# Optimization experiments

Hardware: AMD Instinct MI355X
Metric: run time of the kernel (lower is better)

Reference implementation:

```python
import jax, jax.numpy as jnp
import numpy as np
from jax import lax

DN2 = ('NCHW', 'OIHW', 'NCHW')
DN3 = ('NCDHW', 'OIDHW', 'NCDHW')


def _convlstm_step(h, c, x, W, b):
    # x: [B, Cin, H, W], h/c: [B, nf, H, W], W: [4*nf, Cin+nf, 3, 3]
    comb = jnp.concatenate([x, h], axis=1)
    cc = lax.conv_general_dilated(comb, W, (1, 1), 'SAME', dimension_numbers=DN2)
    cc = cc + b[None, :, None, None]
    ci, cf, co, cg = jnp.split(cc, 4, axis=1)
    i = jax.nn.sigmoid(ci)
    f = jax.nn.sigmoid(cf)
    o = jax.nn.sigmoid(co)
    g = jnp.tanh(cg)
    c_next = f * c + i * g
    h_next = o * jnp.tanh(c_next)
    return h_next, c_next


def setup_inputs() -> dict:
    key = jax.random.key(0)
    ks = jax.random.split(key, 4)
    B, T, Cin, H, W = 32, 12, 1, 64, 64
    nf = 64
    s = 0.05
    return {
        'x': jax.random.normal(ks[0], (B, T, Cin, H, W), jnp.float32),
        'future_step': 12,
        'W_enc': jax.random.normal(ks[1], (4 * nf, Cin + nf, 3, 3), jnp.float32) * s,
        'b_enc': jnp.zeros((4 * nf,), jnp.float32),
        'W_dec': jax.random.normal(ks[2], (4 * nf, nf + nf, 3, 3), jnp.float32) * s,
        'b_dec': jnp.zeros((4 * nf,), jnp.float32),
        'W_cnn': jax.random.normal(ks[3], (1, nf, 1, 3, 3), jnp.float32) * s,
        'b_cnn': jnp.zeros((1,), jnp.float32),
    }


def reference(x, future_step, W_enc, b_enc, W_dec, b_dec, W_cnn, b_cnn):
    B, T, Cin, H, Wd = x.shape
    nf = W_enc.shape[0] // 4
    h0 = jnp.zeros((B, nf, H, Wd), x.dtype)
    c0 = jnp.zeros((B, nf, H, Wd), x.dtype)

    # ---- encoder: scan over time ----
    def enc_step(carry, xt):
        h, c = carry
        h, c = _convlstm_step(h, c, xt, W_enc, b_enc)
        return (h, c), None

    (h_t, _), _ = lax.scan(enc_step, (h0, c0), jnp.moveaxis(x, 1, 0))
    encoder_vector = h_t
    out_encoder_vector = encoder_vector.reshape(B, -1)

    # ---- decoder: feed back h as next input ----
    def dec_step(carry, _):
        ev, h, c = carry
        h, c = _convlstm_step(h, c, ev, W_dec, b_dec)
        return (h, h, c), h

    _, outs = lax.scan(dec_step, (encoder_vector, h0, c0), None, length=future_step)
    # outs: [Tf, B, nf, H, W] -> [B, nf, Tf, H, W]
    outs = jnp.transpose(outs, (1, 2, 0, 3, 4))

    # ---- 3D CNN head: kernel (1,3,3), padding (0,1,1) ----
    y = lax.conv_general_dilated(outs, W_cnn, (1, 1, 1),
                                 [(0, 0), (1, 1), (1, 1)],
                                 dimension_numbers=DN3)
    y = y + b_cnn[None, :, None, None, None]
    # [B, 1, Tf, H, W] -> [B, Tf, 1, H, W]
    y = jnp.transpose(y, (0, 2, 1, 3, 4))
    return y, out_encoder_vector
```

## Files before the change

kernel.cpp:

```cpp
#include <hip/hip_runtime.h>
#include <hip/hip_bf16.h>


#define HW 4096
#define NF 64

typedef __attribute__((ext_vector_type(8))) short bf16x8;
typedef __attribute__((ext_vector_type(4))) float f32x4;

__device__ __forceinline__ float fsig(float v) {
  return __builtin_amdgcn_rcpf(1.f + __expf(-v));
}
__device__ __forceinline__ float ftanh(float v) {
  float vc = fminf(fmaxf(v, -15.f), 15.f);
  float e = __expf(2.f * vc);
  return (e - 1.f) * __builtin_amdgcn_rcpf(e + 1.f);
}
__device__ __forceinline__ float bf2f(short s) {
  union { unsigned u; float f; } a;
  a.u = ((unsigned)(unsigned short)s) << 16;
  return a.f;
}
__device__ __forceinline__ short f2bf(float f) {
  union { float f; unsigned u; } a;
  a.f = f;
  unsigned r = (a.u + 0x7fff + ((a.u >> 16) & 1)) >> 16;
  return (short)r;
}
__device__ __forceinline__ void dma16(const short* g, short* l) {
  __builtin_amdgcn_global_load_lds(
      (const __attribute__((address_space(1))) char*)g,
      (__attribute__((address_space(3))) char*)l, 16, 0, 0);
}

template <bool HAS_X, bool HAS_H, bool FUSE_HEAD>
__global__ __launch_bounds__(512) void lstm_mfma_k(
    const short* __restrict__ hin,
    const short* __restrict__ W,
    const float* __restrict__ wx,
    const float* __restrict__ xpl,
    const float* __restrict__ bias,
    const float* __restrict__ cin,
    const short* __restrict__ zbuf,
    short* __restrict__ hout,
    float* __restrict__ cout,
    const float* __restrict__ wc2,
    const float* __restrict__ bcnn,
    float* __restrict__ yout,
    int th) {
  if (FUSE_HEAD) {
    if (blockIdx.x >= 32) {
      const int f = ((blockIdx.x - 32) * 64 + blockIdx.y) * 512 + threadIdx.x;
      const int pix = f & 4095;
      const int b = f >> 12;
      const int x0 = pix & 63, y0 = pix >> 6;
      float acc = bcnn[0];
      const short* hb = hin + (size_t)b * (HW * 64);
#pragma unroll
      for (int tap = 0; tap < 9; ++tap) {
        const int yy = y0 + tap / 3 - 1, xx = x0 + (tap % 3) - 1;
        if (yy < 0 || yy > 63 || xx < 0 || xx > 63) continue;
        const short* hp = hb + (yy * 64 + xx) * 64;
        const int sw8 = (xx + 1) & 7;
        const float* wp = wc2 + tap * 64;
#pragma unroll
        for (int f8 = 0; f8 < 8; ++f8) {
          bf16x8 v = *reinterpret_cast<const bf16x8*>(hp + ((f8 ^ sw8) * 8));
#pragma unroll
          for (int j = 0; j < 8; ++j)
            acc = fmaf(wp[f8 * 8 + j], bf2f(v[j]), acc);
        }
      }
      yout[(size_t)(b * 12 + th) * HW + pix] = acc;
      return;
    }
  }
  const int b = blockIdx.x;
  const int y = blockIdx.y;
  const int tid = threadIdx.x;
  const int lane = tid & 63;
  const int wv = tid >> 6;
  const int wnf = wv & 3;
  const int whalf = wv >> 2;
  const int col = lane & 15;
  const int quad = lane >> 4;

  __shared__ short As3[3][8192];
  __shared__ short Bs[3 * 66 * 64];
  __shared__ float xs[3][64];

  if (HAS_H) {
    const short* hb = hin + (size_t)b * (HW * 64);
#pragma unroll
    for (int r = 0; r < 3; ++r) {
      const int py = y - 1 + r;
      const short* src = (py >= 0 && py < 64)
          ? hb + ((py * 64 + 8 * wv + (lane >> 3)) * 64 + (lane & 7) * 8)
          : zbuf + lane * 8;
      dma16(src, &Bs[(r * 66 + 8 * wv + 1) * 64]);
    }
#pragma unroll
    for (int k = 0; k < 2; ++k) {
      const short* src = W + (k >> 1) * 16384 + (k & 1) * 8192;
      dma16(src + (wv * 64 + lane) * 8, &As3[k][wv * 64 * 8]);
      dma16(src + (512 + wv * 64 + lane) * 8, &As3[k][(512 + wv * 64) * 8]);
    }
    if (tid < 48) {
      const int r = tid >> 4;
      const int s = ((tid >> 3) & 1) * 65;
      const int ch0 = (tid & 7) * 8;
      bf16x8 z = {0, 0, 0, 0, 0, 0, 0, 0};
      *reinterpret_cast<bf16x8*>(&Bs[(r * 66 + s) * 64 + ch0]) = z;
    }
  }
  if (HAS_X) {
    if (tid < 192) {
      const float* xb = xpl + (size_t)b * (12 * HW);
      const int r = tid >> 6, cx = tid & 63;
      const int py = y - 1 + r;
      xs[r][cx] = (py >= 0 && py < 64) ? xb[py * 64 + cx] : 0.f;
    }
  }
  if (HAS_H) {
    asm volatile("s_waitcnt vmcnt(2) lgkmcnt(0)" ::: "memory");
    __builtin_amdgcn_s_barrier();
  } else {
    __syncthreads();
  }

  f32x4 acc[4][2];
#pragma unroll
  for (int g = 0; g < 4; ++g) {
    const int oc0 = g * 64 + wnf * 16 + quad * 4;
#pragma unroll
    for (int nt = 0; nt < 2; ++nt)
#pragma unroll
      for (int r = 0; r < 4; ++r) acc[g][nt][r] = bias[oc0 + r];
  }

  if (HAS_X) {
#pragma unroll
    for (int tap = 0; tap < 9; ++tap) {
      float xv[2];
#pragma unroll
      for (int nt = 0; nt < 2; ++nt) {
        const int pxx = whalf * 32 + nt * 16 + col + (tap % 3) - 1;
        xv[nt] = (pxx >= 0 && pxx < 64) ? xs[tap / 3][pxx] : 0.f;
      }
      const float* wt = wx + tap * 256;
#pragma unroll
      for (int g = 0; g < 4; ++g) {
        const int oc0 = g * 64 + wnf * 16 + quad * 4;
        const f32x4 w4 = *reinterpret_cast<const f32x4*>(wt + oc0);
#pragma unroll
        for (int nt = 0; nt < 2; ++nt)
#pragma unroll
          for (int r = 0; r < 4; ++r)
            acc[g][nt][r] = fmaf(xv[nt], w4[r], acc[g][nt][r]);
      }
    }
  }

  if (HAS_H) {
    const int axr = (col & 7) << 3;
    bf16x8 bh00, bh01, bh10, bh11;
#pragma unroll
    for (int k = 0; k < 18; ++k) {
      const int tap = k >> 1, gp = k & 1, p = k % 3;
      if (k > 0) {
        if (k == 17)
          asm volatile("s_waitcnt vmcnt(0)" ::: "memory");
        else
          asm volatile("s_waitcnt vmcnt(2)" ::: "memory");
        __builtin_amdgcn_s_barrier();
      }
      if (k + 2 < 18) {
        const int nk = k + 2;
        const short* src = W + (nk >> 1) * 16384 + (nk & 1) * 8192;
        dma16(src + (wv * 64 + lane) * 8, &As3[nk % 3][wv * 64 * 8]);
        dma16(src + (512 + wv * 64 + lane) * 8,
              &As3[nk % 3][(512 + wv * 64) * 8]);
      }
      if (gp == 0) {
        const int hr = tap / 3;
        const int sb = col + tap % 3;
        const int sx = (sb & 7) << 3;
        const int srow = (hr * 66 + whalf * 32 + sb) * 64;
        const int b0 = (srow + quad * 8) ^ sx;
        const int b1 = (srow + 32 + quad * 8) ^ sx;
        bh00 = *reinterpret_cast<const bf16x8*>(&Bs[b0]);
        bh01 = *reinterpret_cast<const bf16x8*>(&Bs[b0 + 1024]);
        bh10 = *reinterpret_cast<const bf16x8*>(&Bs[b1]);
        bh11 = *reinterpret_cast<const bf16x8*>(&Bs[b1 + 1024]);
      }
#pragma unroll
      for (int kc = 0; kc < 2; ++kc) {
        const int chb = kc * 32 + quad * 8;
        const int abase = ((wnf * 16 + col) * 64 + chb) ^ axr;
        bf16x8 a0 = *reinterpret_cast<const bf16x8*>(&As3[p][abase]);
        bf16x8 a1 = *reinterpret_cast<const bf16x8*>(&As3[p][abase + 4096]);
        const bf16x8 bb0 = kc ? bh10 : bh00;
        const bf16x8 bb1 = kc ? bh11 : bh01;
        __builtin_amdgcn_s_setprio(1);
        acc[gp * 2][0] = __builtin_amdgcn_mfma_f32_16x16x32_bf16(a0, bb0, acc[gp * 2][0], 0, 0, 0);
        acc[gp * 2][1] = __builtin_amdgcn_mfma_f32_16x16x32_bf16(a0, bb1, acc[gp * 2][1], 0, 0, 0);
        acc[gp * 2 + 1][0] = __builtin_amdgcn_mfma_f32_16x16x32_bf16(a1, bb0, acc[gp * 2 + 1][0], 0, 0, 0);
        acc[gp * 2 + 1][1] = __builtin_amdgcn_mfma_f32_16x16x32_bf16(a1, bb1, acc[gp * 2 + 1][1], 0, 0, 0);
        __builtin_amdgcn_s_setprio(0);
      }
    }
  }

  const int nf0 = wnf * 16 + quad * 4;
#pragma unroll
  for (int nt = 0; nt < 2; ++nt) {
    const int px = whalf * 32 + nt * 16 + col;
    const int swz = ((px + 1) & 7) << 3;
    const size_t pix = (size_t)b * HW + y * 64 + px;
    f32x4 cold = {0.f, 0.f, 0.f, 0.f};
    if (cin) cold = *reinterpret_cast<const f32x4*>(cin + pix * 64 + nf0);
    f32x4 cnew;
    short hnew[4];
#pragma unroll
    for (int r = 0; r < 4; ++r) {
      float i_ = fsig(acc[0][nt][r]);
      float f_ = fsig(acc[1][nt][r]);
      float o_ = fsig(acc[2][nt][r]);
      float g_ = ftanh(acc[3][nt][r]);
      float cn = fmaf(f_, cold[r], i_ * g_);
      cnew[r] = cn;
      hnew[r] = f2bf(o_ * ftanh(cn));
    }
    *reinterpret_cast<f32x4*>(cout + pix * 64 + nf0) = cnew;
    short4 hv = make_short4(hnew[0], hnew[1], hnew[2], hnew[3]);
    *reinterpret_cast<short4*>(hout + pix * 64 + (nf0 ^ swz)) = hv;
  }
}

__global__ __launch_bounds__(256) void head_k(const short* __restrict__ h,
                                              const float* __restrict__ wc2,
                                              const float* __restrict__ bc,
                                              float* __restrict__ yout, int t) {
  const int tid = blockIdx.x * 256 + threadIdx.x;
  const int pix = tid & 4095;
  const int b = tid >> 12;
  const int x0 = pix & 63, y0 = pix >> 6;
  float acc = bc[0];
  const short* hb = h + (size_t)b * (HW * 64);
#pragma unroll
  for (int tap = 0; tap < 9; ++tap) {
    const int yy = y0 + tap / 3 - 1, xx = x0 + (tap % 3) - 1;
    if (yy < 0 || yy > 63 || xx < 0 || xx > 63) continue;
    const short* hp = hb + (yy * 64 + xx) * 64;
    const int sw8 = (xx + 1) & 7;
    const float* wp = wc2 + tap * 64;
#pragma unroll
    for (int f8 = 0; f8 < 8; ++f8) {
      bf16x8 v = *reinterpret_cast<const bf16x8*>(hp + ((f8 ^ sw8) * 8));
#pragma unroll
      for (int j = 0; j < 8; ++j) acc = fmaf(wp[f8 * 8 + j], bf2f(v[j]), acc);
    }
  }
  yout[(size_t)(b * 12 + t) * HW + pix] = acc;
}

__global__ __launch_bounds__(256) void ev_out_k(const short* __restrict__ h,
                                                float* __restrict__ out) {
  __shared__ float tl[64][65];
  const int b = blockIdx.y, pg = blockIdx.x;
  const int p0 = pg * 64;
  {
    const int pixl = threadIdx.x >> 2, c0 = (threadIdx.x & 3) * 16;
    const int sw8 = (pixl + 1) & 7;
    const short* hp = h + ((size_t)b * HW + p0 + pixl) * 64;
#pragma unroll
    for (int gi = 0; gi < 2; ++gi) {
      const int grp = (c0 >> 3) + gi;
      bf16x8 v = *reinterpret_cast<const bf16x8*>(hp + ((grp ^ sw8) * 8));
#pragma unroll
      for (int j = 0; j < 8; ++j) tl[pixl][grp * 8 + j] = bf2f(v[j]);
    }
  }
  __syncthreads();
  {
    const int ch = threadIdx.x >> 2, q0 = (threadIdx.x & 3) * 16;
    float* op = out + ((size_t)b * 64 + ch) * (size_t)HW + p0 + q0;
#pragma unroll
    for (int i = 0; i < 16; ++i) op[i] = tl[q0 + i][ch];
  }
}

__global__ __launch_bounds__(256) void reo_enc_k(const float* __restrict__ src,
                                                 short* __restrict__ Wh,
                                                 float* __restrict__ wx) {
  const int idx = blockIdx.x * 256 + threadIdx.x;
  if (idx < 9 * 256 * 64) {
    const int tap = idx >> 14, oc = (idx >> 6) & 255, c = idx & 63;
    const int dst = tap * 16384 + (((oc * 64) + c) ^ ((oc & 7) << 3));
    Wh[dst] = f2bf(src[(oc * 65 + (c + 1)) * 9 + tap]);
  }
  if (idx < 256 * 9) {
    const int tap = idx >> 8, oc = idx & 255;
    wx[idx] = src[(oc * 65 + 0) * 9 + tap];
  }
}

__global__ __launch_bounds__(256) void reo_dec_k(const float* __restrict__ src,
                                                 short* __restrict__ Wx,
                                                 short* __restrict__ Ws) {
  const int idx = blockIdx.x * 256 + threadIdx.x;
  if (idx >= 9 * 256 * 64) return;
  const int tap = idx >> 14, oc = (idx >> 6) & 255, c = idx & 63;
  const int dst = tap * 16384 + (((oc * 64) + c) ^ ((oc & 7) << 3));
  const float a = src[(oc * 128 + c) * 9 + tap];
  const float b = src[(oc * 128 + 64 + c) * 9 + tap];
  Wx[dst] = f2bf(a);
  Ws[dst] = f2bf(a + b);
}

__global__ __launch_bounds__(256) void reo_cnn_k(const float* __restrict__ src,
                                                 float* __restrict__ wc2) {
  const int idx = blockIdx.x * 256 + threadIdx.x;
  if (idx >= 576) return;
  wc2[idx] = src[(idx % 64) * 9 + (idx / 64)];
}

extern "C" void kernel_launch(void* const* d_in, const int* in_sizes, int n_in,
                              void* d_out, int out_size, void* d_ws, size_t ws_size,
                              hipStream_t stream) {
  const float* x = (const float*)d_in[0];
  const float* W_enc = (const float*)d_in[2];
  const float* b_enc = (const float*)d_in[3];
  const float* W_dec = (const float*)d_in[4];
  const float* b_dec = (const float*)d_in[5];
  const float* W_cnn = (const float*)d_in[6];
  const float* b_cnn = (const float*)d_in[7];
  float* out = (float*)d_out;
  float* out_y = out;
  float* out_ev = out + 1572864;

  float* ws = (float*)d_ws;
  float* cA = ws;
  float* cB = cA + 8388608;
  short* hA = (short*)(cB + 8388608);
  short* hB = hA + 8388608;
  short* WEh = hB + 8388608;
  short* WDx = WEh + 147456;
  short* WDs = WDx + 147456;
  float* wx = (float*)(WDs + 147456);
  float* wc2 = wx + 2304;
  short* zb = (short*)(wc2 + 576);

  reo_enc_k<<<(147456 + 255) / 256, 256, 0, stream>>>(W_enc, WEh, wx);
  reo_dec_k<<<(147456 + 255) / 256, 256, 0, stream>>>(W_dec, WDx, WDs);
  reo_cnn_k<<<3, 256, 0, stream>>>(W_cnn, wc2);
  hipMemsetAsync(zb, 0, 512 * sizeof(short), stream);

  dim3 gridL(32, 64), blkL(512);
  dim3 gridF(36, 64);
  dim3 gridE(64, 32), blkE(256);

  lstm_mfma_k<true, false, false><<<gridL, blkL, 0, stream>>>(
      nullptr, WEh, wx, x, b_enc, nullptr, zb, hB, cB,
      nullptr, nullptr, nullptr, 0);
  short *ha = hB, *hb = hA;
  float *ca = cB, *cb = cA;

  for (int t = 1; t < 12; ++t) {
    lstm_mfma_k<true, true, false><<<gridL, blkL, 0, stream>>>(
        ha, WEh, wx, x + t * HW, b_enc, ca, zb, hb, cb,
        nullptr, nullptr, nullptr, 0);
    { short* tm = ha; ha = hb; hb = tm; }
    { float* tm = ca; ca = cb; cb = tm; }
  }
  ev_out_k<<<gridE, blkE, 0, stream>>>(ha, out_ev);

  lstm_mfma_k<false, true, false><<<gridL, blkL, 0, stream>>>(
      ha, WDx, nullptr, nullptr, b_dec, nullptr, zb, hb, cb,
      nullptr, nullptr, nullptr, 0);
  { short* tm = ha; ha = hb; hb = tm; }
  { float* tm = ca; ca = cb; cb = tm; }

  for (int t = 1; t < 12; ++t) {
    lstm_mfma_k<false, true, true><<<gridF, blkL, 0, stream>>>(
        ha, WDs, nullptr, nullptr, b_dec, ca, zb, hb, cb,
        wc2, b_cnn, out_y, t - 1);
    { short* tm = ha; ha = hb; hb = tm; }
    { float* tm = ca; ca = cb; cb = tm; }
  }
  head_k<<<512, 256, 0, stream>>>(ha, wc2, b_cnn, out_y, 11);
}
```

Before: 1.815 ms.

## Process eight output rows per block with a rolling h-row ring buffer

Each recurrent LSTM block now computes 8 consecutive image rows instead of 1. It keeps a 4-slot ring buffer of h rows (and x rows) in shared memory, so each input row is loaded once and reused across three output rows rather than reloaded three times. Weight tiles keep streaming through the triple buffer across rows. The grid shrinks from 2048 to 256 blocks, plus 256 head blocks in the fused variant, which cuts redundant halo loads and launch overhead but may leave CUs underused on a 256-CU device. The weights are re-streamed for every row, and the first timestep is split into its own path.

Result: slower. 2.939 ms (+62.0%).

```diff
diff --git a/kernel.cpp b/kernel.cpp
--- a/kernel.cpp
+++ b/kernel.cpp
@@ -48,9 +48,10 @@
     const float* __restrict__ bcnn,
     float* __restrict__ yout,
     int th) {
+  const int tid = threadIdx.x;
   if (FUSE_HEAD) {
-    if (blockIdx.x >= 32) {
-      const int f = ((blockIdx.x - 32) * 64 + blockIdx.y) * 512 + threadIdx.x;
+    if (blockIdx.y >= 8) {
+      const int f = (blockIdx.x + (blockIdx.y - 8) * 32) * 512 + tid;
       const int pix = f & 4095;
       const int b = f >> 12;
       const int x0 = pix & 63, y0 = pix >> 6;
@@ -76,8 +77,6 @@
     }
   }
   const int b = blockIdx.x;
-  const int y = blockIdx.y;
-  const int tid = threadIdx.x;
   const int lane = tid & 63;
   const int wv = tid >> 6;
   const int wnf = wv & 3;
@@ -86,59 +85,27 @@
   const int quad = lane >> 4;
 
   __shared__ short As3[3][8192];
-  __shared__ short Bs[3 * 66 * 64];
-  __shared__ float xs[3][64];
-
-  if (HAS_H) {
-    const short* hb = hin + (size_t)b * (HW * 64);
-#pragma unroll
-    for (int r = 0; r < 3; ++r) {
-      const int py = y - 1 + r;
-      const short* src = (py >= 0 && py < 64)
-          ? hb + ((py * 64 + 8 * wv + (lane >> 3)) * 64 + (lane & 7) * 8)
-          : zbuf + lane * 8;
-      dma16(src, &Bs[(r * 66 + 8 * wv + 1) * 64]);
-    }
-#pragma unroll
-    for (int k = 0; k < 2; ++k) {
-      const short* src = W + (k >> 1) * 16384 + (k & 1) * 8192;
-      dma16(src + (wv * 64 + lane) * 8, &As3[k][wv * 64 * 8]);
-      dma16(src + (512 + wv * 64 + lane) * 8, &As3[k][(512 + wv * 64) * 8]);
-    }
-    if (tid < 48) {
-      const int r = tid >> 4;
-      const int s = ((tid >> 3) & 1) * 65;
-      const int ch0 = (tid & 7) * 8;
-      bf16x8 z = {0, 0, 0, 0, 0, 0, 0, 0};
-      *reinterpret_cast<bf16x8*>(&Bs[(r * 66 + s) * 64 + ch0]) = z;
-    }
-  }
-  if (HAS_X) {
+  __shared__ short Bs[4][4224];
+  __shared__ float xs[4][64];
+
+  if (!HAS_H) {
+    const int y = blockIdx.y;
     if (tid < 192) {
       const float* xb = xpl + (size_t)b * (12 * HW);
       const int r = tid >> 6, cx = tid & 63;
       const int py = y - 1 + r;
       xs[r][cx] = (py >= 0 && py < 64) ? xb[py * 64 + cx] : 0.f;
     }
-  }
-  if (HAS_H) {
-    asm volatile("s_waitcnt vmcnt(2) lgkmcnt(0)" ::: "memory");
-    __builtin_amdgcn_s_barrier();
-  } else {
     __syncthreads();
-  }
-
-  f32x4 acc[4][2];
-#pragma unroll
-  for (int g = 0; g < 4; ++g) {
-    const int oc0 = g * 64 + wnf * 16 + quad * 4;
-#pragma unroll
-    for (int nt = 0; nt < 2; ++nt)
-#pragma unroll
-      for (int r = 0; r < 4; ++r) acc[g][nt][r] = bias[oc0 + r];
-  }
-
-  if (HAS_X) {
+    f32x4 acc[4][2];
+#pragma unroll
+    for (int g = 0; g < 4; ++g) {
+      const int oc0 = g * 64 + wnf * 16 + quad * 4;
+#pragma unroll
+      for (int nt = 0; nt < 2; ++nt)
+#pragma unroll
+        for (int r = 0; r < 4; ++r) acc[g][nt][r] = bias[oc0 + r];
+    }
 #pragma unroll
     for (int tap = 0; tap < 9; ++tap) {
       float xv[2];
@@ -159,46 +126,156 @@
             acc[g][nt][r] = fmaf(xv[nt], w4[r], acc[g][nt][r]);
       }
     }
-  }
-
-  if (HAS_H) {
-    const int axr = (col & 7) << 3;
+    const int nf0 = wnf * 16 + quad * 4;
+#pragma unroll
+    for (int nt = 0; nt < 2; ++nt) {
+      const int px = whalf * 32 + nt * 16 + col;
+      const int swz = ((px + 1) & 7) << 3;
+      const size_t pix = (size_t)b * HW + y * 64 + px;
+      f32x4 cnew;
+      short hnew[4];
+#pragma unroll
+      for (int r = 0; r < 4; ++r) {
+        float i_ = fsig(acc[0][nt][r]);
+        float o_ = fsig(acc[2][nt][r]);
+        float g_ = ftanh(acc[3][nt][r]);
+        float cn = i_ * g_;
+        cnew[r] = cn;
+        hnew[r] = f2bf(o_ * ftanh(cn));
+      }
+      *reinterpret_cast<f32x4*>(cout + pix * 64 + nf0) = cnew;
+      short4 hv = make_short4(hnew[0], hnew[1], hnew[2], hnew[3]);
+      *reinterpret_cast<short4*>(hout + pix * 64 + (nf0 ^ swz)) = hv;
+    }
+    return;
+  }
+
+  const int y0 = blockIdx.y * 8;
+  const short* hb = hin + (size_t)b * (HW * 64);
+  const float* xb = HAS_X ? (xpl + (size_t)b * (12 * HW)) : nullptr;
+
+#pragma unroll
+  for (int r = 0; r < 3; ++r) {
+    const int py = y0 - 1 + r;
+    const short* src = (py >= 0)
+        ? hb + ((py * 64 + 8 * wv + (lane >> 3)) * 64 + (lane & 7) * 8)
+        : zbuf + lane * 8;
+    dma16(src, &Bs[(py + 1) & 3][64 + wv * 512]);
+  }
+#pragma unroll
+  for (int k = 0; k < 2; ++k) {
+    const short* src = W + k * 8192;
+    dma16(src + (wv * 64 + lane) * 8, &As3[k][wv * 64 * 8]);
+    dma16(src + (512 + wv * 64 + lane) * 8, &As3[k][(512 + wv * 64) * 8]);
+  }
+  if (tid < 64) {
+    const int rs = tid >> 4, s = ((tid >> 3) & 1) * 65, ch0 = (tid & 7) * 8;
+    bf16x8 z = {0, 0, 0, 0, 0, 0, 0, 0};
+    *reinterpret_cast<bf16x8*>(&Bs[rs][s * 64 + ch0]) = z;
+  }
+  if (HAS_X) {
+    if (tid < 192) {
+      const int r = tid >> 6, cx = tid & 63;
+      const int py = y0 - 1 + r;
+      xs[(py + 1) & 3][cx] = (py >= 0) ? xb[py * 64 + cx] : 0.f;
+    }
+  }
+  asm volatile("s_waitcnt vmcnt(0) lgkmcnt(0)" ::: "memory");
+  __builtin_amdgcn_s_barrier();
+
+  const int axr = (col & 7) << 3;
+  const int abase0 = ((wnf * 16 + col) * 64 + quad * 8) ^ axr;
+  const int abase1 = ((wnf * 16 + col) * 64 + 32 + quad * 8) ^ axr;
+  short* BsF = &Bs[0][0];
+
+#pragma unroll 1
+  for (int r = 0; r < 8; ++r) {
+    const int y = y0 + r;
+    f32x4 acc[4][2];
+#pragma unroll
+    for (int g = 0; g < 4; ++g) {
+      const int oc0 = g * 64 + wnf * 16 + quad * 4;
+#pragma unroll
+      for (int nt = 0; nt < 2; ++nt)
+#pragma unroll
+        for (int q = 0; q < 4; ++q) acc[g][nt][q] = bias[oc0 + q];
+    }
+    if (HAS_X) {
+#pragma unroll
+      for (int tap = 0; tap < 9; ++tap) {
+        const float* xrow = xs[(y + tap / 3) & 3];
+        float xv[2];
+#pragma unroll
+        for (int nt = 0; nt < 2; ++nt) {
+          const int pxx = whalf * 32 + nt * 16 + col + (tap % 3) - 1;
+          xv[nt] = (pxx >= 0 && pxx < 64) ? xrow[pxx] : 0.f;
+        }
+        const float* wt = wx + tap * 256;
+#pragma unroll
+        for (int g = 0; g < 4; ++g) {
+          const int oc0 = g * 64 + wnf * 16 + quad * 4;
+          const f32x4 w4 = *reinterpret_cast<const f32x4*>(wt + oc0);
+#pragma unroll
+          for (int nt = 0; nt < 2; ++nt)
+#pragma unroll
+            for (int q = 0; q < 4; ++q)
+              acc[g][nt][q] = fmaf(xv[nt], w4[q], acc[g][nt][q]);
+        }
+      }
+    }
+    const int rb[3] = {((y) & 3) * 4224, ((y + 1) & 3) * 4224,
+                       ((y + 2) & 3) * 4224};
     bf16x8 bh00, bh01, bh10, bh11;
-#pragma unroll
-    for (int k = 0; k < 18; ++k) {
-      const int tap = k >> 1, gp = k & 1, p = k % 3;
-      if (k > 0) {
-        if (k == 17)
-          asm volatile("s_waitcnt vmcnt(0)" ::: "memory");
-        else
-          asm volatile("s_waitcnt vmcnt(2)" ::: "memory");
+
+#pragma unroll
+    for (int j = 0; j < 18; ++j) {
+      const int tap = j >> 1, gp = j & 1;
+      if (j == 0) {
         __builtin_amdgcn_s_barrier();
-      }
-      if (k + 2 < 18) {
-        const int nk = k + 2;
-        const short* src = W + (nk >> 1) * 16384 + (nk & 1) * 8192;
-        dma16(src + (wv * 64 + lane) * 8, &As3[nk % 3][wv * 64 * 8]);
+        {
+          const int py = y + 2;
+          const short* srcB = (py <= 63)
+              ? hb + ((py * 64 + 8 * wv + (lane >> 3)) * 64 + (lane & 7) * 8)
+              : zbuf + lane * 8;
+          dma16(srcB, &Bs[(py + 1) & 3][64 + wv * 512]);
+          if (HAS_X) {
+            const short* srcX = (py <= 63)
+                ? reinterpret_cast<const short*>(xb + py * 64 + wv * 8) +
+                      lane * 8
+                : zbuf + lane * 8;
+            if (lane < 2)
+              dma16(srcX, reinterpret_cast<short*>(&xs[(py + 1) & 3][wv * 8]));
+          }
+        }
+      } else if (j == 1) {
+        __builtin_amdgcn_s_barrier();
+      } else {
+        asm volatile("s_waitcnt vmcnt(2)" ::: "memory");
+        __builtin_amdgcn_s_barrier();
+      }
+      {
+        const int p2 = (j + 2) % 18;
+        const short* src = W + (p2 >> 1) * 16384 + (p2 & 1) * 8192;
+        dma16(src + (wv * 64 + lane) * 8, &As3[(j + 2) % 3][wv * 64 * 8]);
         dma16(src + (512 + wv * 64 + lane) * 8,
-              &As3[nk % 3][(512 + wv * 64) * 8]);
+              &As3[(j + 2) % 3][(512 + wv * 64) * 8]);
       }
       if (gp == 0) {
         const int hr = tap / 3;
         const int sb = col + tap % 3;
         const int sx = (sb & 7) << 3;
-        const int srow = (hr * 66 + whalf * 32 + sb) * 64;
-        const int b0 = (srow + quad * 8) ^ sx;
-        const int b1 = (srow + 32 + quad * 8) ^ sx;
-        bh00 = *reinterpret_cast<const bf16x8*>(&Bs[b0]);
-        bh01 = *reinterpret_cast<const bf16x8*>(&Bs[b0 + 1024]);
-        bh10 = *reinterpret_cast<const bf16x8*>(&Bs[b1]);
-        bh11 = *reinterpret_cast<const bf16x8*>(&Bs[b1 + 1024]);
+        const int o = rb[hr] + (whalf * 32 + sb) * 64;
+        bh00 = *reinterpret_cast<const bf16x8*>(&BsF[(o + quad * 8) ^ sx]);
+        bh01 = *reinterpret_cast<const bf16x8*>(&BsF[(o + 1024 + quad * 8) ^ sx]);
+        bh10 = *reinterpret_cast<const bf16x8*>(&BsF[(o + 32 + quad * 8) ^ sx]);
+        bh11 = *reinterpret_cast<const bf16x8*>(&BsF[(o + 1024 + 32 + quad * 8) ^ sx]);
       }
 #pragma unroll
       for (int kc = 0; kc < 2; ++kc) {
-        const int chb = kc * 32 + quad * 8;
-        const int abase = ((wnf * 16 + col) * 64 + chb) ^ axr;
-        bf16x8 a0 = *reinterpret_cast<const bf16x8*>(&As3[p][abase]);
-        bf16x8 a1 = *reinterpret_cast<const bf16x8*>(&As3[p][abase + 4096]);
+        const bf16x8 a0 = *reinterpret_cast<const bf16x8*>(
+            &As3[j % 3][kc ? abase1 : abase0]);
+        const bf16x8 a1 = *reinterpret_cast<const bf16x8*>(
+            &As3[j % 3][(kc ? abase1 : abase0) + 4096]);
         const bf16x8 bb0 = kc ? bh10 : bh00;
         const bf16x8 bb1 = kc ? bh11 : bh01;
         __builtin_amdgcn_s_setprio(1);
@@ -209,31 +286,32 @@
         __builtin_amdgcn_s_setprio(0);
       }
     }
-  }
-
-  const int nf0 = wnf * 16 + quad * 4;
-#pragma unroll
-  for (int nt = 0; nt < 2; ++nt) {
-    const int px = whalf * 32 + nt * 16 + col;
-    const int swz = ((px + 1) & 7) << 3;
-    const size_t pix = (size_t)b * HW + y * 64 + px;
-    f32x4 cold = {0.f, 0.f, 0.f, 0.f};
-    if (cin) cold = *reinterpret_cast<const f32x4*>(cin + pix * 64 + nf0);
-    f32x4 cnew;
-    short hnew[4];
-#pragma unroll
-    for (int r = 0; r < 4; ++r) {
-      float i_ = fsig(acc[0][nt][r]);
-      float f_ = fsig(acc[1][nt][r]);
-      float o_ = fsig(acc[2][nt][r]);
-      float g_ = ftanh(acc[3][nt][r]);
-      float cn = fmaf(f_, cold[r], i_ * g_);
-      cnew[r] = cn;
-      hnew[r] = f2bf(o_ * ftanh(cn));
-    }
-    *reinterpret_cast<f32x4*>(cout + pix * 64 + nf0) = cnew;
-    short4 hv = make_short4(hnew[0], hnew[1], hnew[2], hnew[3]);
-    *reinterpret_cast<short4*>(hout + pix * 64 + (nf0 ^ swz)) = hv;
+
+    const int nf0 = wnf * 16 + quad * 4;
+#pragma unroll
+    for (int nt = 0; nt < 2; ++nt) {
+      const int px = whalf * 32 + nt * 16 + col;
+      const int swz = ((px + 1) & 7) << 3;
+      const size_t pix = (size_t)b * HW + y * 64 + px;
+      f32x4 cold = {0.f, 0.f, 0.f, 0.f};
+      if (cin) cold = *reinterpret_cast<const f32x4*>(cin + pix * 64 + nf0);
+      f32x4 cnew;
+      short hnew[4];
+#pragma unroll
+      for (int q = 0; q < 4; ++q) {
+        float i_ = fsig(acc[0][nt][q]);
+        float f_ = fsig(acc[1][nt][q]);
+        float o_ = fsig(acc[2][nt][q]);
+        float g_ = ftanh(acc[3][nt][q]);
+        float cn = fmaf(f_, cold[q], i_ * g_);
+        cnew[q] = cn;
+        hnew[q] = f2bf(o_ * ftanh(cn));
+      }
+      *reinterpret_cast<f32x4*>(cout + pix * 64 + nf0) = cnew;
+      short4 hv = make_short4(hnew[0], hnew[1], hnew[2], hnew[3]);
+      *reinterpret_cast<short4*>(hout + pix * 64 + (nf0 ^ swz)) = hv;
+    }
+    asm volatile("s_waitcnt vmcnt(0)" ::: "memory");
   }
 }
 
@@ -356,18 +434,20 @@
   reo_cnn_k<<<3, 256, 0, stream>>>(W_cnn, wc2);
   hipMemsetAsync(zb, 0, 512 * sizeof(short), stream);
 
-  dim3 gridL(32, 64), blkL(512);
-  dim3 gridF(36, 64);
+  dim3 blkL(512);
+  dim3 gridT0(32, 64);
+  dim3 gridP(32, 8);
+  dim3 gridF(32, 16);
   dim3 gridE(64, 32), blkE(256);
 
-  lstm_mfma_k<true, false, false><<<gridL, blkL, 0, stream>>>(
+  lstm_mfma_k<true, false, false><<<gridT0, blkL, 0, stream>>>(
       nullptr, WEh, wx, x, b_enc, nullptr, zb, hB, cB,
       nullptr, nullptr, nullptr, 0);
   short *ha = hB, *hb = hA;
   float *ca = cB, *cb = cA;
 
   for (int t = 1; t < 12; ++t) {
-    lstm_mfma_k<true, true, false><<<gridL, blkL, 0, stream>>>(
+    lstm_mfma_k<true, true, false><<<gridP, blkL, 0, stream>>>(
         ha, WEh, wx, x + t * HW, b_enc, ca, zb, hb, cb,
         nullptr, nullptr, nullptr, 0);
     { short* tm = ha; ha = hb; hb = tm; }
@@ -375,7 +455,7 @@
   }
   ev_out_k<<<gridE, blkE, 0, stream>>>(ha, out_ev);
 
-  lstm_mfma_k<false, true, false><<<gridL, blkL, 0, stream>>>(
+  lstm_mfma_k<false, true, false><<<gridP, blkL, 0, stream>>>(
       ha, WDx, nullptr, nullptr, b_dec, nullptr, zb, hb, cb,
       nullptr, nullptr, nullptr, 0);
   { short* tm = ha; ha = hb; hb = tm; }
```
